# Kernel optimization log

Measured on AMD Instinct MI355X. Metric: run time of the kernel, lower is better.

Reference implementation:

```python
import jax, jax.numpy as jnp
import numpy as np
import math

EPS = 1e-6
N_NODES = 25000
N_EDGES = 400000
F = 8            # multivector channels
NB = 8           # blades of Cl(3,0)
NORM_FACTOR = 1.0
SUBSPACES = np.array([1, 3, 3, 1])
REP = np.repeat(np.arange(4), SUBSPACES)   # grade index per blade: [0,1,1,1,2,2,2,3]
GRADES = np.array([0, 1, 1, 1, 2, 2, 2, 3])

def _build_cayley():
    # shortlex blade order for dim 3: 1, e1, e2, e3, e12, e13, e23, e123
    bitmaps = [0, 1, 2, 4, 3, 5, 6, 7]
    b2i = {b: i for i, b in enumerate(bitmaps)}
    def sign(a, b):
        a >>= 1
        s = 0
        while a:
            s += bin(a & b).count('1')
            a >>= 1
        return 1.0 if s % 2 == 0 else -1.0  # euclidean metric (1,1,1)
    C = np.zeros((NB, NB, NB), np.float32)
    for i, bi in enumerate(bitmaps):
        for j, bj in enumerate(bitmaps):
            C[i, b2i[bi ^ bj], j] = sign(bi, bj)   # cayley[left, out, right]
    return C

CAYLEY_NP = _build_cayley()

def _paths():
    p = np.zeros((4, 4, 4), bool)
    for a in range(4):
        for b in range(4):
            for c in range(4):
                blk = CAYLEY_NP[GRADES == a][:, GRADES == b][:, :, GRADES == c]
                p[a, b, c] = np.any(blk != 0)
    return np.nonzero(p)

PI, PJ, PK = _paths()
N_PATHS = len(PI)  # 20 for Cl(3,0)
CAYLEY = jnp.asarray(CAYLEY_NP)

def grade_qs(x):
    # per-grade quadratic form (euclidean: sum of squares), x: [..., 8] -> [..., 4]
    sq = x * x
    return jnp.concatenate([sq[..., 0:1],
                            sq[..., 1:4].sum(-1, keepdims=True),
                            sq[..., 4:7].sum(-1, keepdims=True),
                            sq[..., 7:8]], axis=-1)

def mv_linear(x, w, b=None):
    # w: [out, in, 4] grade-wise weights, repeat-interleaved over blades
    out = jnp.einsum('bmi,nmi->bni', x, w[:, :, REP])
    if b is not None:
        out = out.at[:, :, 0].add(b[0, :, 0])   # bias embedded in scalar blade
    return out

def mv_silu(x, a, b):
    q = grade_qs(x)
    inv = jnp.concatenate([x[..., :1], q[..., 1:]], axis=-1)  # scalar + mag2 per grade
    gate = jax.nn.sigmoid(a * inv + b)[..., REP]
    return gate * x

def sgp(x, w_right, w_geo, w_left, b_left, a_norm):
    # SteerableGeometricProductLayer with NormalizationLayer on the right input
    xr = mv_linear(x, w_right)
    norms = jnp.sqrt(grade_qs(xr))                       # [B,F,4]
    norms = jax.nn.sigmoid(a_norm) * (norms - 1.0) + 1.0
    xr = xr / (norms[..., REP] + EPS)
    W4 = jnp.zeros((F, 4, 4, 4), x.dtype).at[:, PI, PJ, PK].set(w_geo)
    W8 = W4[:, REP][:, :, REP][:, :, :, REP] * CAYLEY    # [F,8,8,8]
    geo = jnp.einsum('bni,nijk,bnk->bnj', x, W8, xr)
    return (mv_linear(x, w_left, b_left) + geo) / math.sqrt(2.0)

def mv_layernorm(x, a):
    n = jnp.sqrt((x * x).sum(-1, keepdims=True)).mean(axis=1, keepdims=True) + EPS
    return a[..., None] * x / n

def block(x, lin_w, lin_b, silu_a, silu_b, gp_wr, gp_w, gp_wl, gp_bl, gp_an, ln_a):
    # CEMLP block: MVLinear -> MVSiLU -> SteerableGeometricProduct -> MVLayerNorm
    x = mv_linear(x, lin_w, lin_b)
    x = mv_silu(x, silu_a, silu_b)
    x = sgp(x, gp_wr, gp_w, gp_wl, gp_bl, gp_an)
    return mv_layernorm(x, ln_a)

def setup_inputs() -> dict:
    key = jax.random.key(0)
    ks = jax.random.split(key, 12)
    h = jax.random.normal(ks[0], (N_NODES, F, NB), jnp.float32)
    edge_index = jax.random.randint(ks[1], (2, N_EDGES), 0, N_NODES)
    def linw(k, out_f, in_f):
        return jax.random.normal(k, (out_f, in_f, 4), jnp.float32) / math.sqrt(in_f)
    inp = dict(h=h, edge_index=edge_index)
    for pref, kk in (('e', 2), ('n', 7)):
        inp[pref + '_lin_w'] = linw(ks[kk], F, 2 * F)
        inp[pref + '_lin_b'] = jnp.zeros((1, F, 1), jnp.float32)
        inp[pref + '_silu_a'] = jnp.ones((1, F, 4), jnp.float32)
        inp[pref + '_silu_b'] = jnp.zeros((1, F, 4), jnp.float32)
        inp[pref + '_gp_wr'] = linw(ks[kk + 1], F, F)
        inp[pref + '_gp_w'] = jax.random.normal(ks[kk + 2], (F, N_PATHS), jnp.float32) / 2.0
        inp[pref + '_gp_wl'] = linw(ks[kk + 3], F, F)
        inp[pref + '_gp_bl'] = jnp.zeros((1, F, 1), jnp.float32)
        inp[pref + '_gp_an'] = jnp.zeros((F, 4), jnp.float32)
        inp[pref + '_ln_a'] = jnp.ones((1, F), jnp.float32)
    return inp

def reference(h, edge_index,
              e_lin_w, e_lin_b, e_silu_a, e_silu_b, e_gp_wr, e_gp_w, e_gp_wl, e_gp_bl, e_gp_an, e_ln_a,
              n_lin_w, n_lin_b, n_silu_a, n_silu_b, n_gp_wr, n_gp_w, n_gp_wl, n_gp_bl, n_gp_an, n_ln_a):
    row, col = edge_index[0], edge_index[1]
    # edge model: gather endpoint features, Clifford MLP block
    m = jnp.concatenate([h[row], h[col]], axis=1)          # [E, 2F, 8]
    m = block(m, e_lin_w, e_lin_b, e_silu_a, e_silu_b,
              e_gp_wr, e_gp_w, e_gp_wl, e_gp_bl, e_gp_an, e_ln_a)
    # unsorted_segment_sum on flattened multivectors, 'sum' aggregation
    agg = jax.ops.segment_sum(m.reshape(N_EDGES, -1), row, num_segments=N_NODES) / NORM_FACTOR
    agg = agg.reshape(N_NODES, F, NB)
    # node update: residual Clifford MLP block on [h, agg]
    upd = jnp.concatenate([h, agg], axis=1)                # [N, 2F, 8]
    upd = block(upd, n_lin_w, n_lin_b, n_silu_a, n_silu_b,
                n_gp_wr, n_gp_w, n_gp_wl, n_gp_bl, n_gp_an, n_ln_a)
    return h + upd
```

## Files before the change

kernel.cpp:

```cpp
#include <hip/hip_runtime.h>

#define NNODES 25000
#define NEDGES 400000
#define EPB 32
#define XSTR2 68
#define EPSF 1e-6f
#define RSQRT2 0.7071067811865476f

typedef _Float16 half8 __attribute__((ext_vector_type(8)));

static constexpr int GJ[64] = {
 0,1,2,3,4,5,6,7,
 1,0,4,5,2,3,7,6,
 2,4,0,6,1,7,3,5,
 3,5,6,0,7,1,2,4,
 4,2,1,7,0,6,5,3,
 5,3,7,1,6,0,4,2,
 6,7,3,2,5,4,0,1,
 7,6,5,4,3,2,1,0};
static constexpr int GS[64] = {
 1, 1, 1, 1, 1, 1, 1, 1,
 1, 1, 1, 1, 1, 1, 1, 1,
 1,-1, 1, 1,-1,-1, 1,-1,
 1,-1,-1, 1, 1,-1,-1, 1,
 1,-1, 1, 1,-1,-1, 1,-1,
 1,-1,-1, 1, 1,-1,-1, 1,
 1, 1,-1, 1,-1, 1,-1,-1,
 1, 1,-1, 1,-1, 1,-1,-1};
static constexpr int GP[64] = {
  0, 1, 1, 1, 2, 2, 2, 3,
  5, 4, 7, 7, 6, 6, 9, 8,
  5, 7, 4, 7, 6, 9, 6, 8,
  5, 7, 7, 4, 9, 6, 6, 8,
 13,11,11,15,10,14,14,12,
 13,11,15,11,14,10,14,12,
 13,15,11,11,14,14,10,12,
 19,18,18,18,17,17,17,16};

struct WP {
  const float *wlin, *blin, *asi, *bsi, *wr, *wg, *wl, *bl, *an, *aln;
};

__device__ __forceinline__ float sigm(float x) {
  return __builtin_amdgcn_rcpf(1.f + __expf(-x));
}
__device__ __forceinline__ float frcp(float x) { return __builtin_amdgcn_rcpf(x); }
__device__ __forceinline__ float fsqrt(float x) { return __builtin_amdgcn_sqrtf(x); }

__device__ __forceinline__ void wave_fence() {
  asm volatile("s_waitcnt lgkmcnt(0)" ::: "memory");
  __builtin_amdgcn_sched_barrier(0);
}

#define C_WR   0
#define C_WL   (C_WR + 288)
#define C_WG   (C_WL + 288)
#define C_BLIN (C_WG + 160)
#define C_ASI  (C_BLIN + 8)
#define C_BSI  (C_ASI + 32)
#define C_BL   (C_BSI + 32)
#define C_AN   (C_BL + 8)
#define C_ALN  (C_AN + 32)
#define C_TOT  (C_ALN + 8)
#define C_WLIN C_TOT
#define CN_TOT (C_WLIN + 8*68)

__device__ __forceinline__ void stage_common(int tid, float* Ws, const WP& wp) {
  int t = tid;
  if (t < 256) Ws[C_WR + (t >> 5) * 36 + (t & 31)] = wp.wr[t];
  if (t < 256) Ws[C_WL + (t >> 5) * 36 + (t & 31)] = wp.wl[t];
  if (t < 160) Ws[C_WG + t] = wp.wg[t];
  if (t < 8)   Ws[C_BLIN + t] = wp.blin[t];
  if (t < 32)  Ws[C_ASI + t] = wp.asi[t];
  if (t < 32)  Ws[C_BSI + t] = wp.bsi[t];
  if (t < 8)   Ws[C_BL + t]  = wp.bl[t];
  if (t < 32)  Ws[C_AN + t]  = wp.an[t];
  if (t < 8)   Ws[C_ALN + t] = wp.aln[t];
}

__device__ __forceinline__ void clifford_tail(float* __restrict__ X,
                                              const float* __restrict__ Ws,
                                              int n, const float* y, float* z)
{
  const float q1 = y[1]*y[1] + y[2]*y[2] + y[3]*y[3];
  const float q2 = y[4]*y[4] + y[5]*y[5] + y[6]*y[6];
  const float q3 = y[7]*y[7];
  const float g0 = sigm(Ws[C_ASI + n*4 + 0] * y[0] + Ws[C_BSI + n*4 + 0]);
  const float g1 = sigm(Ws[C_ASI + n*4 + 1] * q1  + Ws[C_BSI + n*4 + 1]);
  const float g2 = sigm(Ws[C_ASI + n*4 + 2] * q2  + Ws[C_BSI + n*4 + 2]);
  const float g3 = sigm(Ws[C_ASI + n*4 + 3] * q3  + Ws[C_BSI + n*4 + 3]);
  float s[8] = { g0*y[0], g1*y[1], g1*y[2], g1*y[3],
                 g2*y[4], g2*y[5], g2*y[6], g3*y[7] };
  *(float4*)&X[n*8]     = make_float4(s[0], s[1], s[2], s[3]);
  *(float4*)&X[n*8 + 4] = make_float4(s[4], s[5], s[6], s[7]);
  wave_fence();

  float xr[8], zl[8];
  #pragma unroll
  for (int i = 0; i < 8; ++i) { xr[i] = 0.f; zl[i] = 0.f; }
  #pragma unroll
  for (int m = 0; m < 8; ++m) {
    const float4 wr4 = *(const float4*)&Ws[C_WR + n * 36 + m * 4];
    const float4 wl4 = *(const float4*)&Ws[C_WL + n * 36 + m * 4];
    const float4 xa = *(const float4*)&X[m * 8];
    const float4 xb = *(const float4*)&X[m * 8 + 4];
    xr[0]=fmaf(xa.x,wr4.x,xr[0]); xr[1]=fmaf(xa.y,wr4.y,xr[1]); xr[2]=fmaf(xa.z,wr4.y,xr[2]); xr[3]=fmaf(xa.w,wr4.y,xr[3]);
    xr[4]=fmaf(xb.x,wr4.z,xr[4]); xr[5]=fmaf(xb.y,wr4.z,xr[5]); xr[6]=fmaf(xb.z,wr4.z,xr[6]); xr[7]=fmaf(xb.w,wr4.w,xr[7]);
    zl[0]=fmaf(xa.x,wl4.x,zl[0]); zl[1]=fmaf(xa.y,wl4.y,zl[1]); zl[2]=fmaf(xa.z,wl4.y,zl[2]); zl[3]=fmaf(xa.w,wl4.y,zl[3]);
    zl[4]=fmaf(xb.x,wl4.z,zl[4]); zl[5]=fmaf(xb.y,wl4.z,zl[5]); zl[6]=fmaf(xb.z,wl4.z,zl[6]); zl[7]=fmaf(xb.w,wl4.w,zl[7]);
  }
  zl[0] += Ws[C_BL + n];

  {
    const float t0 = fabsf(xr[0]);
    const float t1 = fsqrt(xr[1]*xr[1] + xr[2]*xr[2] + xr[3]*xr[3]);
    const float t2 = fsqrt(xr[4]*xr[4] + xr[5]*xr[5] + xr[6]*xr[6]);
    const float t3 = fabsf(xr[7]);
    const float d0 = frcp(sigm(Ws[C_AN + n*4 + 0]) * (t0 - 1.f) + 1.f + EPSF);
    const float d1 = frcp(sigm(Ws[C_AN + n*4 + 1]) * (t1 - 1.f) + 1.f + EPSF);
    const float d2 = frcp(sigm(Ws[C_AN + n*4 + 2]) * (t2 - 1.f) + 1.f + EPSF);
    const float d3 = frcp(sigm(Ws[C_AN + n*4 + 3]) * (t3 - 1.f) + 1.f + EPSF);
    xr[0] *= d0; xr[1] *= d1; xr[2] *= d1; xr[3] *= d1;
    xr[4] *= d2; xr[5] *= d2; xr[6] *= d2; xr[7] *= d3;
  }

  float geo[8];
  #pragma unroll
  for (int i = 0; i < 8; ++i) geo[i] = 0.f;
  {
    const int wgb = C_WG + n * 20;
    #pragma unroll
    for (int i = 0; i < 8; ++i) {
      #pragma unroll
      for (int k = 0; k < 8; ++k) {
        const float t = s[i] * xr[k];
        const float w = Ws[wgb + GP[i * 8 + k]];
        geo[GJ[i * 8 + k]] = fmaf(GS[i * 8 + k] > 0 ? w : -w, t, geo[GJ[i * 8 + k]]);
      }
    }
  }

  #pragma unroll
  for (int i = 0; i < 8; ++i) z[i] = (zl[i] + geo[i]) * RSQRT2;

  float sq = 0.f;
  #pragma unroll
  for (int i = 0; i < 8; ++i) sq = fmaf(z[i], z[i], sq);
  float nr = fsqrt(sq);
  nr += __shfl_xor(nr, 1);
  nr += __shfl_xor(nr, 2);
  nr += __shfl_xor(nr, 4);
  const float scale = Ws[C_ALN + n] * frcp(nr * 0.125f + EPSF);
  #pragma unroll
  for (int i = 0; i < 8; ++i) z[i] *= scale;
}

__global__ __launch_bounds__(1024)
void csr_scan_fast(const int* __restrict__ deg, int* __restrict__ ptr,
                   int* __restrict__ fill)
{
  __shared__ int wsum[16];
  const int t = threadIdx.x;
  const int base = t * 32;
  int d[32];
  int s = 0;
  #pragma unroll
  for (int i = 0; i < 8; ++i) {
    int idx = base + i * 4;
    int4 v = make_int4(0, 0, 0, 0);
    if (idx + 3 < NNODES) v = *(const int4*)(deg + idx);
    else {
      if (idx + 0 < NNODES) v.x = deg[idx + 0];
      if (idx + 1 < NNODES) v.y = deg[idx + 1];
      if (idx + 2 < NNODES) v.z = deg[idx + 2];
    }
    d[i*4+0] = v.x; d[i*4+1] = v.y; d[i*4+2] = v.z; d[i*4+3] = v.w;
    s += v.x + v.y + v.z + v.w;
  }
  const int lane = t & 63;
  int incl = s;
  #pragma unroll
  for (int off = 1; off < 64; off <<= 1) {
    int u = __shfl_up(incl, off);
    if (lane >= off) incl += u;
  }
  const int wv = t >> 6;
  if (lane == 63) wsum[wv] = incl;
  __syncthreads();
  if (t < 16) {
    int v = wsum[t];
    int inc = v;
    #pragma unroll
    for (int off = 1; off < 16; off <<= 1) {
      int u = __shfl_up(inc, off);
      if (t >= off) inc += u;
    }
    wsum[t] = inc - v;
  }
  __syncthreads();
  int run = wsum[wv] + (incl - s);
  #pragma unroll
  for (int i = 0; i < 8; ++i) {
    int idx = base + i * 4;
    int4 pv;
    pv.x = run; run += d[i*4+0];
    pv.y = run; run += d[i*4+1];
    pv.z = run; run += d[i*4+2];
    pv.w = run; run += d[i*4+3];
    if (idx + 3 < NNODES) {
      *(int4*)(ptr + idx)  = pv;
      *(int4*)(fill + idx) = pv;
    } else {
      if (idx + 0 < NNODES) { ptr[idx+0] = pv.x; fill[idx+0] = pv.x; }
      if (idx + 1 < NNODES) { ptr[idx+1] = pv.y; fill[idx+1] = pv.y; }
      if (idx + 2 < NNODES) { ptr[idx+2] = pv.z; fill[idx+2] = pv.z; }
    }
  }
  if (t == 1023) ptr[NNODES] = NEDGES;
}

#define PRE_BLOCKS ((NNODES + EPB - 1) / EPB)
#define CNT_BLOCKS ((NEDGES + 255) / 256)

__global__ __launch_bounds__(256)
void pre_count(const float* __restrict__ h,
               const float* __restrict__ wle,
               float* __restrict__ ue, float* __restrict__ ve,
               const int* __restrict__ eidx, int* __restrict__ deg)
{
  __shared__ __align__(16) float We[8 * 68];
  __shared__ __align__(16) float Xs[EPB * XSTR2];
  const int tid = threadIdx.x;

  if (blockIdx.x >= PRE_BLOCKS) {
    int e = (blockIdx.x - PRE_BLOCKS) * 256 + tid;
    if (e < NEDGES) atomicAdd(&deg[eidx[e]], 1);
    return;
  }

  for (int t = tid; t < 512; t += 256) We[(t >> 6) * 68 + (t & 63)] = wle[t];
  const int el = tid >> 3, n = tid & 7;
  const int item = blockIdx.x * EPB + el;
  float* X = &Xs[el * XSTR2];
  const bool act = item < NNODES;
  if (act) {
    const float4* ph = (const float4*)(h + (size_t)item * 64 + n * 8);
    *(float4*)&X[n * 8]     = ph[0];
    *(float4*)&X[n * 8 + 4] = ph[1];
  }
  __syncthreads();
  if (!act) return;
  float ua[8], va[8];
  #pragma unroll
  for (int i = 0; i < 8; ++i) { ua[i] = 0.f; va[i] = 0.f; }
  #pragma unroll
  for (int m = 0; m < 8; ++m) {
    const float4 xa = *(const float4*)&X[m * 8];
    const float4 xb = *(const float4*)&X[m * 8 + 4];
    const float4 wa = *(const float4*)&We[n * 68 + m * 4];
    const float4 wb = *(const float4*)&We[n * 68 + (m + 8) * 4];
    ua[0]=fmaf(xa.x,wa.x,ua[0]); ua[1]=fmaf(xa.y,wa.y,ua[1]); ua[2]=fmaf(xa.z,wa.y,ua[2]); ua[3]=fmaf(xa.w,wa.y,ua[3]);
    ua[4]=fmaf(xb.x,wa.z,ua[4]); ua[5]=fmaf(xb.y,wa.z,ua[5]); ua[6]=fmaf(xb.z,wa.z,ua[6]); ua[7]=fmaf(xb.w,wa.w,ua[7]);
    va[0]=fmaf(xa.x,wb.x,va[0]); va[1]=fmaf(xa.y,wb.y,va[1]); va[2]=fmaf(xa.z,wb.y,va[2]); va[3]=fmaf(xa.w,wb.y,va[3]);
    va[4]=fmaf(xb.x,wb.z,va[4]); va[5]=fmaf(xb.y,wb.z,va[5]); va[6]=fmaf(xb.z,wb.z,va[6]); va[7]=fmaf(xb.w,wb.w,va[7]);
  }
  float4* pu = (float4*)(ue + (size_t)item * 64 + n * 8);
  pu[0] = make_float4(ua[0],ua[1],ua[2],ua[3]); pu[1] = make_float4(ua[4],ua[5],ua[6],ua[7]);
  float4* pv = (float4*)(ve + (size_t)item * 64 + n * 8);
  pv[0] = make_float4(va[0],va[1],va[2],va[3]); pv[1] = make_float4(va[4],va[5],va[6],va[7]);
}

#define EDGE_BLOCKS4 (NEDGES / EPB)
#define SCT_BLOCKS4  ((NEDGES + 255) / 256)

__global__ __launch_bounds__(256)
void cgenn4_edge_scatter(const int* __restrict__ eidx,
                         const float* __restrict__ ue, const float* __restrict__ ve,
                         int* __restrict__ fill, int* __restrict__ elist,
                         _Float16* __restrict__ msgh, WP wp)
{
  __shared__ __align__(16) float Ws[C_TOT];
  __shared__ __align__(16) float Xs[EPB * XSTR2];
  const int tid = threadIdx.x;

  if (blockIdx.x >= EDGE_BLOCKS4) {
    int e = (blockIdx.x - EDGE_BLOCKS4) * 256 + tid;
    if (e < NEDGES) {
      int pos = atomicAdd(&fill[eidx[e]], 1);
      elist[pos] = e;
    }
    return;
  }

  const int el = tid >> 3, n = tid & 7;
  const int e = blockIdx.x * EPB + el;

  const int r = eidx[e];
  const int c = eidx[NEDGES + e];
  const float4* pu = (const float4*)(ue + (size_t)r * 64 + n * 8);
  const float4 u0 = pu[0], u1 = pu[1];
  const float4* pv = (const float4*)(ve + (size_t)c * 64 + n * 8);
  const float4 v0 = pv[0], v1 = pv[1];

  stage_common(tid, Ws, wp);
  __syncthreads();

  float y[8] = { u0.x+v0.x, u0.y+v0.y, u0.z+v0.z, u0.w+v0.w,
                 u1.x+v1.x, u1.y+v1.y, u1.z+v1.z, u1.w+v1.w };
  y[0] += Ws[C_BLIN + n];

  float z[8];
  clifford_tail(&Xs[el * XSTR2], Ws, n, y, z);

  half8 hm;
  hm[0]=(_Float16)z[0]; hm[1]=(_Float16)z[1]; hm[2]=(_Float16)z[2]; hm[3]=(_Float16)z[3];
  hm[4]=(_Float16)z[4]; hm[5]=(_Float16)z[5]; hm[6]=(_Float16)z[6]; hm[7]=(_Float16)z[7];
  *(half8*)(msgh + (size_t)e * 64 + n * 8) = hm;
}

#define NPB 4
__global__ __launch_bounds__(256)
void cgenn4_node(const float* __restrict__ h,
                 const _Float16* __restrict__ msgh,
                 const int* __restrict__ ptr,
                 const int* __restrict__ elist,
                 float* __restrict__ out, WP wp)
{
  __shared__ __align__(16) float Ws[CN_TOT];
  __shared__ __align__(16) float Xs[NPB * 132];
  const int tid  = threadIdx.x;
  const int wv   = tid >> 6;
  const int slot = (tid >> 3) & 7;
  const int n    = tid & 7;
  const int nid  = blockIdx.x * NPB + wv;
  float* X = &Xs[wv * 132];

  stage_common(tid, Ws, wp);
  for (int t = tid; t < 512; t += 256)
    Ws[C_WLIN + (t >> 6) * 68 + (t & 63)] = wp.wlin[t];

  const int beg = ptr[nid], end = ptr[nid + 1];

  float a[8];
  #pragma unroll
  for (int i = 0; i < 8; ++i) a[i] = 0.f;
  const _Float16* mb = msgh + (size_t)n * 8;
  int p = beg + slot;
  int e0 = (p < end) ? elist[p] : 0;
  while (p < end) {
    const int pn = p + 8;
    const int e1 = (pn < end) ? elist[pn] : 0;
    const half8 m = *(const half8*)(mb + (size_t)e0 * 64);
    #pragma unroll
    for (int i = 0; i < 8; ++i) a[i] += (float)m[i];
    e0 = e1; p = pn;
  }
  #pragma unroll
  for (int i = 0; i < 8; ++i) {
    a[i] += __shfl_xor(a[i], 8);
    a[i] += __shfl_xor(a[i], 16);
    a[i] += __shfl_xor(a[i], 32);
  }

  __syncthreads();

  if (slot == 0) {
    float hr[8];
    const float4* ph = (const float4*)(h + (size_t)nid * 64 + n * 8);
    const float4 h0 = ph[0], h1 = ph[1];
    hr[0]=h0.x; hr[1]=h0.y; hr[2]=h0.z; hr[3]=h0.w;
    hr[4]=h1.x; hr[5]=h1.y; hr[6]=h1.z; hr[7]=h1.w;
    *(float4*)&X[n*8]         = h0;
    *(float4*)&X[n*8 + 4]     = h1;
    *(float4*)&X[(8+n)*8]     = make_float4(a[0], a[1], a[2], a[3]);
    *(float4*)&X[(8+n)*8 + 4] = make_float4(a[4], a[5], a[6], a[7]);
    wave_fence();

    float y[8];
    #pragma unroll
    for (int i = 0; i < 8; ++i) y[i] = 0.f;
    #pragma unroll
    for (int m = 0; m < 16; ++m) {
      const float4 w4 = *(const float4*)&Ws[C_WLIN + n * 68 + m * 4];
      const float4 xa = *(const float4*)&X[m * 8];
      const float4 xb = *(const float4*)&X[m * 8 + 4];
      y[0]=fmaf(xa.x,w4.x,y[0]); y[1]=fmaf(xa.y,w4.y,y[1]); y[2]=fmaf(xa.z,w4.y,y[2]); y[3]=fmaf(xa.w,w4.y,y[3]);
      y[4]=fmaf(xb.x,w4.z,y[4]); y[5]=fmaf(xb.y,w4.z,y[5]); y[6]=fmaf(xb.z,w4.z,y[6]); y[7]=fmaf(xb.w,w4.w,y[7]);
    }
    y[0] += Ws[C_BLIN + n];

    float z[8];
    clifford_tail(X, Ws, n, y, z);

    float4* po = (float4*)(out + (size_t)nid * 64 + n * 8);
    po[0] = make_float4(hr[0]+z[0], hr[1]+z[1], hr[2]+z[2], hr[3]+z[3]);
    po[1] = make_float4(hr[4]+z[4], hr[5]+z[5], hr[6]+z[6], hr[7]+z[7]);
  }
}

#define XSTR 132
#define O_WLIN 0
#define O_BLIN (O_WLIN + 8*68)
#define O_ASI  (O_BLIN + 8)
#define O_BSI  (O_ASI + 32)
#define O_WR   (O_BSI + 32)
#define O_WG   (O_WR + 8*36)
#define O_WL   (O_WG + 160)
#define O_BL   (O_WL + 8*36)
#define O_AN   (O_BL + 8)
#define O_ALN  (O_AN + 32)
#define W_TOT  (O_ALN + 8)

template<bool IS_NODE>
__global__ __launch_bounds__(256)
void cgenn_block(const float* __restrict__ h,
                 const int* __restrict__ eidx,
                 float* agg_out, WP wp)
{
  __shared__ __align__(16) float Ws[W_TOT];
  __shared__ __align__(16) float Xs[EPB * XSTR];
  const int tid = threadIdx.x;
  for (int t = tid; t < 512; t += 256) Ws[O_WLIN + (t >> 6) * 68 + (t & 63)] = wp.wlin[t];
  { int t = tid;
    if (t < 256) Ws[O_WR + (t >> 5) * 36 + (t & 31)] = wp.wr[t];
    if (t < 256) Ws[O_WL + (t >> 5) * 36 + (t & 31)] = wp.wl[t];
    if (t < 160) Ws[O_WG + t] = wp.wg[t];
    if (t < 8)   Ws[O_BLIN + t] = wp.blin[t];
    if (t < 32)  Ws[O_ASI + t] = wp.asi[t];
    if (t < 32)  Ws[O_BSI + t] = wp.bsi[t];
    if (t < 8)   Ws[O_BL + t] = wp.bl[t];
    if (t < 32)  Ws[O_AN + t] = wp.an[t];
    if (t < 8)   Ws[O_ALN + t] = wp.aln[t];
  }
  const int el = tid >> 3;
  const int n  = tid & 7;
  const int item = blockIdx.x * EPB + el;
  float* X = &Xs[el * XSTR];
  bool active = true;
  int r = 0;
  float hr[8];
  if (IS_NODE) {
    active = (item < NNODES);
    if (active) {
      const float4* ph = (const float4*)(h + (size_t)item * 64 + n * 8);
      float4 a0 = ph[0], a1 = ph[1];
      hr[0]=a0.x; hr[1]=a0.y; hr[2]=a0.z; hr[3]=a0.w;
      hr[4]=a1.x; hr[5]=a1.y; hr[6]=a1.z; hr[7]=a1.w;
      *(float4*)&X[n*8]     = a0;
      *(float4*)&X[n*8 + 4] = a1;
      const float4* pa = (const float4*)(agg_out + (size_t)item * 64 + n * 8);
      *(float4*)&X[(8+n)*8]     = pa[0];
      *(float4*)&X[(8+n)*8 + 4] = pa[1];
    }
  } else {
    r = eidx[item];
    const int c = eidx[NEDGES + item];
    const float4* ph = (const float4*)(h + (size_t)r * 64 + n * 8);
    float4 a0 = ph[0], a1 = ph[1];
    const float4* pc = (const float4*)(h + (size_t)c * 64 + n * 8);
    float4 b0 = pc[0], b1 = pc[1];
    *(float4*)&X[n*8]       = a0;  *(float4*)&X[n*8 + 4]     = a1;
    *(float4*)&X[(8+n)*8]   = b0;  *(float4*)&X[(8+n)*8 + 4] = b1;
  }
  __syncthreads();
  float y[8];
  #pragma unroll
  for (int i = 0; i < 8; ++i) y[i] = 0.f;
  #pragma unroll
  for (int m = 0; m < 16; ++m) {
    const float4 w4 = *(const float4*)&Ws[O_WLIN + n * 68 + m * 4];
    const float4 xa = *(const float4*)&X[m * 8];
    const float4 xb = *(const float4*)&X[m * 8 + 4];
    y[0]=fmaf(xa.x,w4.x,y[0]); y[1]=fmaf(xa.y,w4.y,y[1]); y[2]=fmaf(xa.z,w4.y,y[2]); y[3]=fmaf(xa.w,w4.y,y[3]);
    y[4]=fmaf(xb.x,w4.z,y[4]); y[5]=fmaf(xb.y,w4.z,y[5]); y[6]=fmaf(xb.z,w4.z,y[6]); y[7]=fmaf(xb.w,w4.w,y[7]);
  }
  y[0] += Ws[O_BLIN + n];
  float z[8];
  clifford_tail(X, Ws, n, y, z);
  if (IS_NODE) {
    if (active) {
      float4* po = (float4*)(agg_out + (size_t)item * 64 + n * 8);
      po[0] = make_float4(hr[0]+z[0], hr[1]+z[1], hr[2]+z[2], hr[3]+z[3]);
      po[1] = make_float4(hr[4]+z[4], hr[5]+z[5], hr[6]+z[6], hr[7]+z[7]);
    }
  } else {
    float* dst = agg_out + (size_t)r * 64 + n * 8;
    #pragma unroll
    for (int i = 0; i < 8; ++i) atomicAdd(dst + i, z[i]);
  }
}

extern "C" void kernel_launch(void* const* d_in, const int* in_sizes, int n_in,
                              void* d_out, int out_size, void* d_ws, size_t ws_size,
                              hipStream_t stream)
{
  (void)in_sizes; (void)n_in; (void)out_size;
  const float* h   = (const float*)d_in[0];
  const int* eidx  = (const int*)d_in[1];
  WP we = { (const float*)d_in[2],  (const float*)d_in[3],  (const float*)d_in[4],
            (const float*)d_in[5],  (const float*)d_in[6],  (const float*)d_in[7],
            (const float*)d_in[8],  (const float*)d_in[9],  (const float*)d_in[10],
            (const float*)d_in[11] };
  WP wn = { (const float*)d_in[12], (const float*)d_in[13], (const float*)d_in[14],
            (const float*)d_in[15], (const float*)d_in[16], (const float*)d_in[17],
            (const float*)d_in[18], (const float*)d_in[19], (const float*)d_in[20],
            (const float*)d_in[21] };
  float* out = (float*)d_out;

  const size_t mhsz   = (size_t)NEDGES * 64 * sizeof(_Float16);
  const size_t nodef  = (size_t)NNODES * 64 * sizeof(float);
  const size_t elsz   = (size_t)NEDGES * sizeof(int);
  const size_t degsz  = (size_t)25008 * sizeof(int);
  const size_t fillsz = (size_t)25008 * sizeof(int);
  const size_t need   = mhsz + 2 * nodef + elsz + degsz + fillsz;

  if (ws_size >= need) {
    char* base = (char*)d_ws;
    _Float16* msgh = (_Float16*)base;   base += mhsz;
    float* ue   = (float*)base;         base += nodef;
    float* ve   = (float*)base;         base += nodef;
    int* elist  = (int*)base;           base += elsz;
    int* deg    = (int*)base;           base += degsz;
    int* fill   = (int*)base;

    hipMemsetAsync(deg, 0, (NNODES + 1) * sizeof(int), stream);
    pre_count<<<dim3(PRE_BLOCKS + CNT_BLOCKS), dim3(256), 0, stream>>>(
        h, we.wlin, ue, ve, eidx, deg);
    csr_scan_fast<<<dim3(1), dim3(1024), 0, stream>>>(deg, deg, fill);
    cgenn4_edge_scatter<<<dim3(EDGE_BLOCKS4 + SCT_BLOCKS4), dim3(256), 0, stream>>>(
        eidx, ue, ve, fill, elist, msgh, we);
    cgenn4_node<<<dim3(NNODES / NPB), dim3(256), 0, stream>>>(
        h, msgh, deg, elist, out, wn);
  } else {
    hipMemsetAsync(d_out, 0, (size_t)NNODES * 64 * sizeof(float), stream);
    cgenn_block<false><<<dim3(NEDGES / EPB), dim3(256), 0, stream>>>(h, eidx, out, we);
    cgenn_block<true><<<dim3((NNODES + EPB - 1) / EPB), dim3(256), 0, stream>>>(h, eidx, out, wn);
  }
}
```

Before: 159.9 us.

## Process edges in CSR-sorted order so node aggregation reads messages contiguously

A separate scatter kernel now writes (row,col) pairs into CSR order. The edge kernel then runs over sorted positions and writes messages at those positions. The node kernel therefore reads its messages contiguously and no longer needs the elist indirection, which removes random 128B gathers from the aggregation. In exchange, the scatter becomes a serial dependency before the edge kernel instead of overlapping with it, and the fallback path is refactored to share the weight staging.

Measured after the change: 153.2 us. 1.04x faster.

```diff
diff --git a/kernel.cpp b/kernel.cpp
--- a/kernel.cpp
+++ b/kernel.cpp
@@ -270,36 +270,33 @@
   pv[0] = make_float4(va[0],va[1],va[2],va[3]); pv[1] = make_float4(va[4],va[5],va[6],va[7]);
 }
 
-#define EDGE_BLOCKS4 (NEDGES / EPB)
-#define SCT_BLOCKS4  ((NEDGES + 255) / 256)
+__global__ __launch_bounds__(256) void csr_scatter_pairs(const int* __restrict__ eidx,
+                                                         int* __restrict__ fill,
+                                                         int2* __restrict__ ers) {
+  int e = blockIdx.x * 256 + threadIdx.x;
+  if (e < NEDGES) {
+    const int r = eidx[e];
+    const int c = eidx[NEDGES + e];
+    int pos = atomicAdd(&fill[r], 1);
+    ers[pos] = make_int2(r, c);
+  }
+}
 
 __global__ __launch_bounds__(256)
-void cgenn4_edge_scatter(const int* __restrict__ eidx,
-                         const float* __restrict__ ue, const float* __restrict__ ve,
-                         int* __restrict__ fill, int* __restrict__ elist,
-                         _Float16* __restrict__ msgh, WP wp)
+void cgenn5_edge(const int2* __restrict__ ers,
+                 const float* __restrict__ ue, const float* __restrict__ ve,
+                 _Float16* __restrict__ msgh, WP wp)
 {
   __shared__ __align__(16) float Ws[C_TOT];
   __shared__ __align__(16) float Xs[EPB * XSTR2];
   const int tid = threadIdx.x;
-
-  if (blockIdx.x >= EDGE_BLOCKS4) {
-    int e = (blockIdx.x - EDGE_BLOCKS4) * 256 + tid;
-    if (e < NEDGES) {
-      int pos = atomicAdd(&fill[eidx[e]], 1);
-      elist[pos] = e;
-    }
-    return;
-  }
-
   const int el = tid >> 3, n = tid & 7;
-  const int e = blockIdx.x * EPB + el;
-
-  const int r = eidx[e];
-  const int c = eidx[NEDGES + e];
-  const float4* pu = (const float4*)(ue + (size_t)r * 64 + n * 8);
+  const int p = blockIdx.x * EPB + el;
+
+  const int2 rc = ers[p];
+  const float4* pu = (const float4*)(ue + (size_t)rc.x * 64 + n * 8);
   const float4 u0 = pu[0], u1 = pu[1];
-  const float4* pv = (const float4*)(ve + (size_t)c * 64 + n * 8);
+  const float4* pv = (const float4*)(ve + (size_t)rc.y * 64 + n * 8);
   const float4 v0 = pv[0], v1 = pv[1];
 
   stage_common(tid, Ws, wp);
@@ -315,15 +312,14 @@
   half8 hm;
   hm[0]=(_Float16)z[0]; hm[1]=(_Float16)z[1]; hm[2]=(_Float16)z[2]; hm[3]=(_Float16)z[3];
   hm[4]=(_Float16)z[4]; hm[5]=(_Float16)z[5]; hm[6]=(_Float16)z[6]; hm[7]=(_Float16)z[7];
-  *(half8*)(msgh + (size_t)e * 64 + n * 8) = hm;
+  *(half8*)(msgh + (size_t)p * 64 + n * 8) = hm;
 }
 
 #define NPB 4
 __global__ __launch_bounds__(256)
-void cgenn4_node(const float* __restrict__ h,
+void cgenn5_node(const float* __restrict__ h,
                  const _Float16* __restrict__ msgh,
                  const int* __restrict__ ptr,
-                 const int* __restrict__ elist,
                  float* __restrict__ out, WP wp)
 {
   __shared__ __align__(16) float Ws[CN_TOT];
@@ -345,15 +341,10 @@
   #pragma unroll
   for (int i = 0; i < 8; ++i) a[i] = 0.f;
   const _Float16* mb = msgh + (size_t)n * 8;
-  int p = beg + slot;
-  int e0 = (p < end) ? elist[p] : 0;
-  while (p < end) {
-    const int pn = p + 8;
-    const int e1 = (pn < end) ? elist[pn] : 0;
-    const half8 m = *(const half8*)(mb + (size_t)e0 * 64);
+  for (int p = beg + slot; p < end; p += 8) {
+    const half8 m = *(const half8*)(mb + (size_t)p * 64);
     #pragma unroll
     for (int i = 0; i < 8; ++i) a[i] += (float)m[i];
-    e0 = e1; p = pn;
   }
   #pragma unroll
   for (int i = 0; i < 8; ++i) {
@@ -398,44 +389,22 @@
   }
 }
 
-#define XSTR 132
-#define O_WLIN 0
-#define O_BLIN (O_WLIN + 8*68)
-#define O_ASI  (O_BLIN + 8)
-#define O_BSI  (O_ASI + 32)
-#define O_WR   (O_BSI + 32)
-#define O_WG   (O_WR + 8*36)
-#define O_WL   (O_WG + 160)
-#define O_BL   (O_WL + 8*36)
-#define O_AN   (O_BL + 8)
-#define O_ALN  (O_AN + 32)
-#define W_TOT  (O_ALN + 8)
-
 template<bool IS_NODE>
 __global__ __launch_bounds__(256)
 void cgenn_block(const float* __restrict__ h,
                  const int* __restrict__ eidx,
                  float* agg_out, WP wp)
 {
-  __shared__ __align__(16) float Ws[W_TOT];
-  __shared__ __align__(16) float Xs[EPB * XSTR];
+  __shared__ __align__(16) float Ws[CN_TOT];
+  __shared__ __align__(16) float Xs[EPB * 132];
   const int tid = threadIdx.x;
-  for (int t = tid; t < 512; t += 256) Ws[O_WLIN + (t >> 6) * 68 + (t & 63)] = wp.wlin[t];
-  { int t = tid;
-    if (t < 256) Ws[O_WR + (t >> 5) * 36 + (t & 31)] = wp.wr[t];
-    if (t < 256) Ws[O_WL + (t >> 5) * 36 + (t & 31)] = wp.wl[t];
-    if (t < 160) Ws[O_WG + t] = wp.wg[t];
-    if (t < 8)   Ws[O_BLIN + t] = wp.blin[t];
-    if (t < 32)  Ws[O_ASI + t] = wp.asi[t];
-    if (t < 32)  Ws[O_BSI + t] = wp.bsi[t];
-    if (t < 8)   Ws[O_BL + t] = wp.bl[t];
-    if (t < 32)  Ws[O_AN + t] = wp.an[t];
-    if (t < 8)   Ws[O_ALN + t] = wp.aln[t];
-  }
+  stage_common(tid, Ws, wp);
+  for (int t = tid; t < 512; t += 256)
+    Ws[C_WLIN + (t >> 6) * 68 + (t & 63)] = wp.wlin[t];
   const int el = tid >> 3;
   const int n  = tid & 7;
   const int item = blockIdx.x * EPB + el;
-  float* X = &Xs[el * XSTR];
+  float* X = &Xs[el * 132];
   bool active = true;
   int r = 0;
   float hr[8];
@@ -468,13 +437,13 @@
   for (int i = 0; i < 8; ++i) y[i] = 0.f;
   #pragma unroll
   for (int m = 0; m < 16; ++m) {
-    const float4 w4 = *(const float4*)&Ws[O_WLIN + n * 68 + m * 4];
+    const float4 w4 = *(const float4*)&Ws[C_WLIN + n * 68 + m * 4];
     const float4 xa = *(const float4*)&X[m * 8];
     const float4 xb = *(const float4*)&X[m * 8 + 4];
     y[0]=fmaf(xa.x,w4.x,y[0]); y[1]=fmaf(xa.y,w4.y,y[1]); y[2]=fmaf(xa.z,w4.y,y[2]); y[3]=fmaf(xa.w,w4.y,y[3]);
     y[4]=fmaf(xb.x,w4.z,y[4]); y[5]=fmaf(xb.y,w4.z,y[5]); y[6]=fmaf(xb.z,w4.z,y[6]); y[7]=fmaf(xb.w,w4.w,y[7]);
   }
-  y[0] += Ws[O_BLIN + n];
+  y[0] += Ws[C_BLIN + n];
   float z[8];
   clifford_tail(X, Ws, n, y, z);
   if (IS_NODE) {
@@ -509,17 +478,17 @@
 
   const size_t mhsz   = (size_t)NEDGES * 64 * sizeof(_Float16);
   const size_t nodef  = (size_t)NNODES * 64 * sizeof(float);
-  const size_t elsz   = (size_t)NEDGES * sizeof(int);
+  const size_t pairsz = (size_t)NEDGES * sizeof(int2);
   const size_t degsz  = (size_t)25008 * sizeof(int);
   const size_t fillsz = (size_t)25008 * sizeof(int);
-  const size_t need   = mhsz + 2 * nodef + elsz + degsz + fillsz;
+  const size_t need   = mhsz + 2 * nodef + pairsz + degsz + fillsz;
 
   if (ws_size >= need) {
     char* base = (char*)d_ws;
     _Float16* msgh = (_Float16*)base;   base += mhsz;
     float* ue   = (float*)base;         base += nodef;
     float* ve   = (float*)base;         base += nodef;
-    int* elist  = (int*)base;           base += elsz;
+    int2* ers   = (int2*)base;          base += pairsz;
     int* deg    = (int*)base;           base += degsz;
     int* fill   = (int*)base;
 
@@ -527,10 +496,9 @@
     pre_count<<<dim3(PRE_BLOCKS + CNT_BLOCKS), dim3(256), 0, stream>>>(
         h, we.wlin, ue, ve, eidx, deg);
     csr_scan_fast<<<dim3(1), dim3(1024), 0, stream>>>(deg, deg, fill);
-    cgenn4_edge_scatter<<<dim3(EDGE_BLOCKS4 + SCT_BLOCKS4), dim3(256), 0, stream>>>(
-        eidx, ue, ve, fill, elist, msgh, we);
-    cgenn4_node<<<dim3(NNODES / NPB), dim3(256), 0, stream>>>(
-        h, msgh, deg, elist, out, wn);
+    csr_scatter_pairs<<<dim3(CNT_BLOCKS), dim3(256), 0, stream>>>(eidx, fill, ers);
+    cgenn5_edge<<<dim3(NEDGES / EPB), dim3(256), 0, stream>>>(ers, ue, ve, msgh, we);
+    cgenn5_node<<<dim3(NNODES / NPB), dim3(256), 0, stream>>>(h, msgh, deg, out, wn);
   } else {
     hipMemsetAsync(d_out, 0, (size_t)NNODES * 64 * sizeof(float), stream);
     cgenn_block<false><<<dim3(NEDGES / EPB), dim3(256), 0, stream>>>(h, eidx, out, we);
```
